# Kernel tuning notes

Measured on AMD Instinct MI355X. Metric: run time of the kernel, lower is better.

Reference implementation:

```python
import jax, jax.numpy as jnp
import numpy as np

# ---- module configuration (from init_kwargs) ----
NX, NV = 2048, 1024
LX = 1.0
VMAX = 6.0
DX = LX / NX
DV = 2.0 * VMAX / NV
XS = jnp.linspace(-LX / 2 + DX / 2, LX / 2 - DX / 2, NX)
VS = jnp.linspace(-VMAX + DV / 2, VMAX - DV / 2, NV)
AE, AI = 1.0, 1836.0
ZE, ZI = -1.0, 1.0
OMEGA_C_TAU = 1.0
NU_EE, NU_II = 1.0, 0.1
DT = 1e-3
T_LBO = 1.0  # LBO temperature, u = 0


def minmod(a, b):
    return jnp.where(a * b > 0, jnp.sign(a) * jnp.minimum(jnp.abs(a), jnp.abs(b)), 0.0)


def _sl(a, lo, hi, axis):
    return jax.lax.slice_in_dim(a, lo, hi, axis=axis)


def slope_limited_flux_divergence(f_pad, F, dx, axis):
    # f_pad has N+4 cells along `axis` (2 ghost cells per side). MUSCL + minmod.
    n = f_pad.shape[axis]
    d = _sl(f_pad, 1, n, axis) - _sl(f_pad, 0, n - 1, axis)          # n-1 diffs
    sigma = minmod(_sl(d, 0, n - 2, axis), _sl(d, 1, n - 1, axis))    # slopes for cells 1..n-2
    fc = _sl(f_pad, 1, n - 1, axis)                                   # cells 1..n-2
    m = n - 2
    fL = _sl(fc, 0, m - 1, axis) + 0.5 * _sl(sigma, 0, m - 1, axis)   # left interface states
    fR = _sl(fc, 1, m, axis) - 0.5 * _sl(sigma, 1, m, axis)           # right interface states
    flux = F(fL, fR)                                                  # N+1 interface fluxes
    k = flux.shape[axis]
    return (_sl(flux, 1, k, axis) - _sl(flux, 0, k - 1, axis)) / dx   # N cells


def pad_x_periodic(f):
    return jnp.concatenate([f[-2:, :], f, f[:2, :]], axis=0)


def pad_v_zero(f):
    z = jnp.zeros((f.shape[0], 2), f.dtype)
    return jnp.concatenate([z, f, z], axis=1)


def poisson_solve(rho_c):
    # dE/dx = rho_c, zero-mean E (periodic-compatible gauge)
    E = jnp.cumsum(rho_c) * DX
    return E - jnp.mean(E)


def species_rhs(f, E, A, Z):
    v = VS[None, :]
    Fx = lambda l, r: jnp.where(v > 0, l * v, r * v)                  # upwind in x
    vdfdx = slope_limited_flux_divergence(pad_x_periodic(f), Fx, DX, axis=0)
    Ec = (OMEGA_C_TAU * Z / A) * E[:, None]
    Fv = lambda l, r: jnp.where(Ec > 0, l * Ec, r * Ec)               # upwind in v
    Edfdv = slope_limited_flux_divergence(pad_v_zero(f), Fv, DV, axis=1)
    return -vdfdx - Edfdv


def vlasov_rhs(fe, fi):
    ne = jnp.sum(fe, axis=1) * DV
    ni = jnp.sum(fi, axis=1) * DV
    E = poisson_solve(ZE * ne + ZI * ni)
    return species_rhs(fe, E, AE, ZE), species_rhs(fi, E, AI, ZI)


def ssprk2(fe, fi, dt):
    re, ri = vlasov_rhs(fe, fi)
    fe1, fi1 = fe + dt * re, fi + dt * ri
    re1, ri1 = vlasov_rhs(fe1, fi1)
    return 0.5 * (fe + fe1 + dt * re1), 0.5 * (fi + fi1 + dt * ri1)


def lbo_diagonals(lam):
    # L f = lam * d/dv( v f + T df/dv ), central differences
    vm = jnp.roll(VS, 1)
    vp = jnp.roll(VS, -1)
    dl = lam * (T_LBO / DV**2 - vm / (2 * DV))
    du = lam * (T_LBO / DV**2 + vp / (2 * DV))
    d = lam * (-2.0 * T_LBO / DV**2) * jnp.ones(NV, XS.dtype)
    return dl.at[0].set(0.0), d, du.at[-1].set(0.0)


def nu_shape():
    midpt = LX / 3
    ef = LX / 6 / 10
    h0 = lambda x: 1 + jnp.exp(x / ef - midpt / ef)
    return 1.0 / (0.5 * (h0(XS) + h0(-XS)))  # [Nx]


def thomas(dl, d, du, b):
    # Thomas algorithm; dl[0]==0 and du[-1]==0 assumed.
    def fwd(carry, inp):
        cp, bp = carry
        dli, di, dui, bi = inp
        m = di - dli * cp
        cpi = dui / m
        bpi = (bi - dli * bp) / m
        return (cpi, bpi), (cpi, bpi)
    z = jnp.zeros((), b.dtype)
    _, (cp, bp) = jax.lax.scan(fwd, (z, z), (dl, d, du, b))
    def bwd(x_next, inp):
        cpi, bpi = inp
        x = bpi - cpi * x_next
        return x, x
    _, x = jax.lax.scan(bwd, z, (cp, bp), reverse=True)
    return x


def implicit_collide(f, lam, dt):
    dl, d, du = lbo_diagonals(lam)
    nu = nu_shape()
    def solve_row(nui, frow):
        return thomas(-dt * nui * dl, 1.0 - dt * nui * d, -dt * nui * du, frow)
    return jax.vmap(solve_row)(nu, f)


def setup_inputs() -> dict:
    key = jax.random.key(0)
    k1, k2 = jax.random.split(key)
    fe = jax.random.uniform(k1, (NX, NV), dtype=jnp.float32)
    fi = jax.random.uniform(k2, (NX, NV), dtype=jnp.float32)
    return {"fe": fe, "fi": fi}


def reference(fe, fi):
    fe1, fi1 = ssprk2(fe, fi, DT)
    fe2 = implicit_collide(fe1, NU_EE, DT)
    fi2 = implicit_collide(fi1, NU_II, DT)
    return jnp.stack([fe2, fi2])  # [2, Nx, Nv]
```

## Files before the change

kernel.cpp:

```cpp
#include <hip/hip_runtime.h>
#include <math.h>

#define NX 2048
#define NV 1024

static constexpr float DXf    = 1.0f / 2048.0f;
static constexpr float DVf    = 12.0f / 1024.0f;
static constexpr float DTf    = 0.001f;
static constexpr float INV_DX = 2048.0f;
static constexpr float INV_DV = 1024.0f / 12.0f;

__device__ __forceinline__ float minmod_f(float a, float b) {
    return __builtin_amdgcn_fmed3f(a, b, 0.0f);
}

__device__ __forceinline__ float frcp(float x) {
    return __builtin_amdgcn_rcpf(x);
}

__device__ __forceinline__ int swz2048(int x) {
    return ((x & 7) << 8) + (x >> 3);
}
__device__ __forceinline__ int swz512(int x) {
    return ((x & 7) << 6) + (x >> 3);
}

__device__ __forceinline__ void rhs4(const float* __restrict__ g, int i, int j0, float Ecs,
                                     float4& f0v, float4& rv) {
    const float* rowc = g + i * NV;
    const float* rm1  = g + (((i - 1) & (NX - 1)) * NV);
    const float* rm2  = g + (((i - 2) & (NX - 1)) * NV);
    const float* rp1  = g + (((i + 1) & (NX - 1)) * NV);
    const float* rp2  = g + (((i + 2) & (NX - 1)) * NV);

    float4 c   = *(const float4*)(rowc + j0);
    float4 xm1 = *(const float4*)(rm1 + j0);
    float4 xm2 = *(const float4*)(rm2 + j0);
    float4 xp1 = *(const float4*)(rp1 + j0);
    float4 xp2 = *(const float4*)(rp2 + j0);
    float4 lm = make_float4(0.f, 0.f, 0.f, 0.f);
    float4 rp = make_float4(0.f, 0.f, 0.f, 0.f);
    if (j0 >= 4)      lm = *(const float4*)(rowc + j0 - 4);
    if (j0 <= NV - 8) rp = *(const float4*)(rowc + j0 + 4);

    float vals[8] = {lm.z, lm.w, c.x, c.y, c.z, c.w, rp.x, rp.y};
    const float* cc   = (const float*)&c;
    const float* am1  = (const float*)&xm1;
    const float* am2  = (const float*)&xm2;
    const float* ap1  = (const float*)&xp1;
    const float* ap2  = (const float*)&xp2;
    float* f0o = (float*)&f0v;
    float* ro  = (float*)&rv;

    #pragma unroll
    for (int k = 0; k < 4; ++k) {
        float f0  = cc[k];
        float fm1 = am1[k], fm2 = am2[k], fp1 = ap1[k], fp2 = ap2[k];

        float vx = (DVf * ((float)(j0 + k) + 0.5f) - 6.0f) * INV_DX;
        float dm1 = fm1 - fm2, d0 = f0 - fm1, dp1 = fp1 - f0, dp2 = fp2 - fp1;
        float sm1 = minmod_f(dm1, d0);
        float s0  = minmod_f(d0, dp1);
        float sp1 = minmod_f(dp1, dp2);
        float selx = (vx > 0.0f) ? (d0 + 0.5f * (s0 - sm1))
                                 : (dp1 - 0.5f * (sp1 - s0));
        float vdfdx = vx * selx;

        float gm2 = vals[k], gm1 = vals[k + 1], gp1 = vals[k + 3], gp2 = vals[k + 4];
        float em1 = gm1 - gm2, e0 = f0 - gm1, ep1 = gp1 - f0, ep2 = gp2 - gp1;
        float tm1 = minmod_f(em1, e0);
        float t0  = minmod_f(e0, ep1);
        float tp1 = minmod_f(ep1, ep2);
        float selv = (Ecs > 0.0f) ? (e0 + 0.5f * (t0 - tm1))
                                  : (ep1 - 0.5f * (tp1 - t0));
        float Edfdv = Ecs * selv;

        f0o[k] = f0;
        ro[k]  = -vdfdx - Edfdv;
    }
}

__global__ __launch_bounds__(256) void moments_kernel(const float* __restrict__ fe,
                                                      const float* __restrict__ fi,
                                                      float* __restrict__ se,
                                                      float* __restrict__ si) {
    const int g = swz512(blockIdx.x);
    const int t = threadIdx.x, lane = t & 63, wv = t >> 6;
    const int row = (g << 2) + wv;
    const float* rpe = fe + (size_t)row * NV;
    const float* rpi = fi + (size_t)row * NV;
    float a = 0.0f, b = 0.0f;
    #pragma unroll
    for (int q = 0; q < 4; ++q) {
        float4 x = *(const float4*)(rpe + 4 * lane + 256 * q);
        float4 y = *(const float4*)(rpi + 4 * lane + 256 * q);
        a += x.x + x.y + x.z + x.w;
        b += y.x + y.y + y.z + y.w;
    }
    #pragma unroll
    for (int off = 32; off > 0; off >>= 1) {
        a += __shfl_down(a, off, 64);
        b += __shfl_down(b, off, 64);
    }
    if (lane == 0) { se[row] = a; si[row] = b; }
}

__global__ __launch_bounds__(256) void escan_kernel(const float* __restrict__ se_,
                                                    const float* __restrict__ si_,
                                                    float* __restrict__ E) {
    const int t = threadIdx.x, lane = t & 63, wv = t >> 6;
    const int k0 = t * 8;
    float4 a0 = *(const float4*)(se_ + k0);
    float4 a1 = *(const float4*)(se_ + k0 + 4);
    float4 b0 = *(const float4*)(si_ + k0);
    float4 b1 = *(const float4*)(si_ + k0 + 4);
    float rho[8];
    rho[0] = DVf * (b0.x - a0.x); rho[1] = DVf * (b0.y - a0.y);
    rho[2] = DVf * (b0.z - a0.z); rho[3] = DVf * (b0.w - a0.w);
    rho[4] = DVf * (b1.x - a1.x); rho[5] = DVf * (b1.y - a1.y);
    rho[6] = DVf * (b1.z - a1.z); rho[7] = DVf * (b1.w - a1.w);
    float s = 0.0f, w = 0.0f;
    #pragma unroll
    for (int r = 0; r < 8; ++r) {
        s += rho[r];
        w += rho[r] * (float)(NX - (k0 + r));
    }
    float sc = s;
    #pragma unroll
    for (int off = 1; off < 64; off <<= 1) {
        float u = __shfl_up(sc, off, 64);
        if (lane >= off) sc += u;
    }
    #pragma unroll
    for (int off = 32; off > 0; off >>= 1) w += __shfl_down(w, off, 64);
    __shared__ float wsum[4], wtot[4];
    if (lane == 63) wsum[wv] = sc;
    if (lane == 0)  wtot[wv] = w;
    __syncthreads();
    float base = 0.0f;
    #pragma unroll
    for (int u = 0; u < 4; ++u) if (u < wv) base += wsum[u];
    float W = wtot[0] + wtot[1] + wtot[2] + wtot[3];
    float run = base + sc - s;
    const float mean = W * (1.0f / (float)NX);
    #pragma unroll
    for (int r = 0; r < 8; ++r) {
        run += rho[r];
        E[k0 + r] = DXf * (run - mean);
    }
}

__global__ __launch_bounds__(256) void stage1_kernel(const float* __restrict__ fe,
                                                     const float* __restrict__ fi,
                                                     const float* __restrict__ E0,
                                                     float* __restrict__ fe1,
                                                     float* __restrict__ fi1,
                                                     float* __restrict__ se1,
                                                     float* __restrict__ si1) {
    const int row = swz2048(blockIdx.x);
    const int sp  = blockIdx.y;
    const float* f = sp ? fi : fe;
    float* f1 = sp ? fi1 : fe1;
    const float zoa = sp ? (1.0f / 1836.0f) : -1.0f;
    const float Ecs = zoa * E0[row] * INV_DV;
    const int t = threadIdx.x, lane = t & 63, wv = t >> 6;
    const int j0 = 4 * t;

    float4 f0v, rv;
    rhs4(f, row, j0, Ecs, f0v, rv);
    float4 o;
    o.x = f0v.x + DTf * rv.x;
    o.y = f0v.y + DTf * rv.y;
    o.z = f0v.z + DTf * rv.z;
    o.w = f0v.w + DTf * rv.w;
    *(float4*)(f1 + (size_t)row * NV + j0) = o;

    float s = o.x + o.y + o.z + o.w;
    #pragma unroll
    for (int off = 32; off > 0; off >>= 1) s += __shfl_down(s, off, 64);
    __shared__ float sred[4];
    if (lane == 0) sred[wv] = s;
    __syncthreads();
    if (t == 0) (sp ? si1 : se1)[row] = sred[0] + sred[1] + sred[2] + sred[3];
}

__global__ __launch_bounds__(256) void stage2_rhs_kernel(const float* __restrict__ fe,
                                                         const float* __restrict__ fi,
                                                         const float* __restrict__ fe1,
                                                         const float* __restrict__ fi1,
                                                         const float* __restrict__ E1,
                                                         float* __restrict__ out) {
    const int row = swz2048(blockIdx.x);
    const int sp  = blockIdx.y;
    const float* h  = sp ? fi : fe;
    const float* f1 = sp ? fi1 : fe1;
    const float zoa = sp ? (1.0f / 1836.0f) : -1.0f;
    const float Ecs = zoa * E1[row] * INV_DV;
    const int t = threadIdx.x;
    const int j0 = 4 * t;
    float* orow = out + ((size_t)sp * NX + row) * NV;

    float4 f0v, rv;
    rhs4(f1, row, j0, Ecs, f0v, rv);
    float4 h4 = *(const float4*)(h + (size_t)row * NV + j0);
    float4 o;
    o.x = 0.5f * h4.x + 0.5f * f0v.x + (0.5f * DTf) * rv.x;
    o.y = 0.5f * h4.y + 0.5f * f0v.y + (0.5f * DTf) * rv.y;
    o.z = 0.5f * h4.z + 0.5f * f0v.z + (0.5f * DTf) * rv.z;
    o.w = 0.5f * h4.w + 0.5f * f0v.w + (0.5f * DTf) * rv.w;
    *(float4*)(orow + j0) = o;
}

__global__ __launch_bounds__(256) void collide_kernel(float* __restrict__ out) {
    const int g  = swz512(blockIdx.x);
    const int sp = blockIdx.y;
    const int t = threadIdx.x, lane = t & 63, wv = t >> 6;
    const int row = (g << 2) + wv;
    const float lam = sp ? 0.1f : 1.0f;
    float* orow = out + ((size_t)sp * NX + row) * NV;

    const float Tdv2   = 1.0f / (DVf * DVf);
    const float inv2dv = 0.5f / DVf;
    const float xi = DXf * ((float)row + 0.5f) - 0.5f;
    const float nu = 1.0f / (1.0f + 0.5f * (expf(60.0f * xi - 20.0f) + expf(-60.0f * xi - 20.0f)));
    const float K = DTf * nu * lam;
    const float b = 1.0f + 2.0f * K * Tdv2;

    const int j0 = 16 * lane;

    float4 q0 = *(const float4*)(orow + j0);
    float4 q1 = *(const float4*)(orow + j0 + 4);
    float4 q2 = *(const float4*)(orow + j0 + 8);
    float4 q3 = *(const float4*)(orow + j0 + 12);
    float d[16] = {q0.x, q0.y, q0.z, q0.w, q1.x, q1.y, q1.z, q1.w,
                   q2.x, q2.y, q2.z, q2.w, q3.x, q3.y, q3.z, q3.w};

    float Dv[16], Av[16], Cv[16];
    #pragma unroll
    for (int r = 0; r < 16; ++r) {
        const int j = j0 + r;
        float a = (j == 0)      ? 0.0f : -K * (Tdv2 - (DVf * ((float)j - 0.5f) - 6.0f) * inv2dv);
        float c = (j == NV - 1) ? 0.0f : -K * (Tdv2 + (DVf * ((float)j + 1.5f) - 6.0f) * inv2dv);
        if (r == 0) {
            float e = frcp(b);
            Dv[0] = e * d[0];
            Av[0] = e * a;
            Cv[0] = e * c;
        } else {
            float e = frcp(b - a * Cv[r - 1]);
            Dv[r] = e * (d[r] - a * Dv[r - 1]);
            Av[r] = -e * a * Av[r - 1];
            Cv[r] = e * c;
        }
    }
    #pragma unroll
    for (int r = 14; r >= 0; --r) {
        Dv[r] = Dv[r] - Cv[r] * Dv[r + 1];
        Av[r] = Av[r] - Cv[r] * Av[r + 1];
        Cv[r] = -Cv[r] * Cv[r + 1];
    }

    float la = Av[0],  ra = Cv[0],  d0 = Dv[0];
    float lb = Av[15], rb = Cv[15], d1 = Dv[15];
    #pragma unroll
    for (int s = 1; s < 64; s <<= 1) {
        float lb_m = __shfl_up(lb, s, 64);
        float rb_m = __shfl_up(rb, s, 64);
        float d1_m = __shfl_up(d1, s, 64);
        if (lane < s) { lb_m = 0.0f; rb_m = 0.0f; d1_m = 0.0f; }
        float la_p = __shfl_down(la, s, 64);
        float ra_p = __shfl_down(ra, s, 64);
        float d0_p = __shfl_down(d0, s, 64);
        if (lane + s > 63) { la_p = 0.0f; ra_p = 0.0f; d0_p = 0.0f; }

        float m00 = 1.0f - la * rb_m;
        float m01 = -ra * la_p;
        float m10 = -lb * rb_m;
        float m11 = 1.0f - rb * la_p;
        float idet = frcp(m00 * m11 - m01 * m10);

        float Lr0 = -la * lb_m, Lr1 = -lb * lb_m;
        float Rr0 = -ra * ra_p, Rr1 = -rb * ra_p;
        float e0 = d0 - la * d1_m - ra * d0_p;
        float e1 = d1 - lb * d1_m - rb * d0_p;

        la = idet * (m11 * Lr0 - m01 * Lr1);
        lb = idet * (m00 * Lr1 - m10 * Lr0);
        ra = idet * (m11 * Rr0 - m01 * Rr1);
        rb = idet * (m00 * Rr1 - m10 * Rr0);
        d0 = idet * (m11 * e0 - m01 * e1);
        d1 = idet * (m00 * e1 - m10 * e0);
    }
    float zl = __shfl_up(d1, 1, 64);
    if (lane == 0) zl = 0.0f;
    float yr = __shfl_down(d0, 1, 64);
    if (lane == 63) yr = 0.0f;

    #pragma unroll
    for (int r = 0; r < 16; ++r) Dv[r] = Dv[r] - Av[r] * zl - Cv[r] * yr;
    #pragma unroll
    for (int q = 0; q < 4; ++q) {
        float4 o;
        o.x = Dv[4 * q + 0];
        o.y = Dv[4 * q + 1];
        o.z = Dv[4 * q + 2];
        o.w = Dv[4 * q + 3];
        *(float4*)(orow + j0 + 4 * q) = o;
    }
}

extern "C" void kernel_launch(void* const* d_in, const int* in_sizes, int n_in,
                              void* d_out, int out_size, void* d_ws, size_t ws_size,
                              hipStream_t stream) {
    const float* fe = (const float*)d_in[0];
    const float* fi = (const float*)d_in[1];
    float* out = (float*)d_out;
    const size_t P = (size_t)NX * NV;

    float* fe1 = (float*)d_ws;
    float* fi1 = fe1 + P;
    float* se  = fi1 + P;
    float* si  = se + NX;
    float* se1 = si + NX;
    float* si1 = se1 + NX;
    float* E0  = si1 + NX;
    float* E1  = E0 + NX;

    dim3 rgrid(2048, 2);
    dim3 qgrid(512, 2);

    moments_kernel<<<512, 256, 0, stream>>>(fe, fi, se, si);
    escan_kernel<<<1, 256, 0, stream>>>(se, si, E0);
    stage1_kernel<<<rgrid, 256, 0, stream>>>(fe, fi, E0, fe1, fi1, se1, si1);
    escan_kernel<<<1, 256, 0, stream>>>(se1, si1, E1);
    stage2_rhs_kernel<<<rgrid, 256, 0, stream>>>(fe, fi, fe1, fi1, E1, out);
    collide_kernel<<<qgrid, 256, 0, stream>>>(out);
}
```

Measured before the change: 105.1 us.

## Fold E-field scan into stage kernels by per-block recomputation of prefix sums

Removes the two single-block escan launches. Each stage block now recomputes its own row's E value from the full 2048-entry moment arrays, using a masked reduction for the prefix and a weighted sum for the mean. This trades two serialized tiny kernels and their launch gaps for redundant reads and reductions of 16 KB in each of 4096 blocks per stage, plus an extra __syncthreads. It also switches expf to __expf in the collision coefficient.

```diff
diff --git a/kernel.cpp b/kernel.cpp
--- a/kernel.cpp
+++ b/kernel.cpp
@@ -25,89 +25,9 @@
     return ((x & 7) << 6) + (x >> 3);
 }
 
-__device__ __forceinline__ void rhs4(const float* __restrict__ g, int i, int j0, float Ecs,
-                                     float4& f0v, float4& rv) {
-    const float* rowc = g + i * NV;
-    const float* rm1  = g + (((i - 1) & (NX - 1)) * NV);
-    const float* rm2  = g + (((i - 2) & (NX - 1)) * NV);
-    const float* rp1  = g + (((i + 1) & (NX - 1)) * NV);
-    const float* rp2  = g + (((i + 2) & (NX - 1)) * NV);
-
-    float4 c   = *(const float4*)(rowc + j0);
-    float4 xm1 = *(const float4*)(rm1 + j0);
-    float4 xm2 = *(const float4*)(rm2 + j0);
-    float4 xp1 = *(const float4*)(rp1 + j0);
-    float4 xp2 = *(const float4*)(rp2 + j0);
-    float4 lm = make_float4(0.f, 0.f, 0.f, 0.f);
-    float4 rp = make_float4(0.f, 0.f, 0.f, 0.f);
-    if (j0 >= 4)      lm = *(const float4*)(rowc + j0 - 4);
-    if (j0 <= NV - 8) rp = *(const float4*)(rowc + j0 + 4);
-
-    float vals[8] = {lm.z, lm.w, c.x, c.y, c.z, c.w, rp.x, rp.y};
-    const float* cc   = (const float*)&c;
-    const float* am1  = (const float*)&xm1;
-    const float* am2  = (const float*)&xm2;
-    const float* ap1  = (const float*)&xp1;
-    const float* ap2  = (const float*)&xp2;
-    float* f0o = (float*)&f0v;
-    float* ro  = (float*)&rv;
-
-    #pragma unroll
-    for (int k = 0; k < 4; ++k) {
-        float f0  = cc[k];
-        float fm1 = am1[k], fm2 = am2[k], fp1 = ap1[k], fp2 = ap2[k];
-
-        float vx = (DVf * ((float)(j0 + k) + 0.5f) - 6.0f) * INV_DX;
-        float dm1 = fm1 - fm2, d0 = f0 - fm1, dp1 = fp1 - f0, dp2 = fp2 - fp1;
-        float sm1 = minmod_f(dm1, d0);
-        float s0  = minmod_f(d0, dp1);
-        float sp1 = minmod_f(dp1, dp2);
-        float selx = (vx > 0.0f) ? (d0 + 0.5f * (s0 - sm1))
-                                 : (dp1 - 0.5f * (sp1 - s0));
-        float vdfdx = vx * selx;
-
-        float gm2 = vals[k], gm1 = vals[k + 1], gp1 = vals[k + 3], gp2 = vals[k + 4];
-        float em1 = gm1 - gm2, e0 = f0 - gm1, ep1 = gp1 - f0, ep2 = gp2 - gp1;
-        float tm1 = minmod_f(em1, e0);
-        float t0  = minmod_f(e0, ep1);
-        float tp1 = minmod_f(ep1, ep2);
-        float selv = (Ecs > 0.0f) ? (e0 + 0.5f * (t0 - tm1))
-                                  : (ep1 - 0.5f * (tp1 - t0));
-        float Edfdv = Ecs * selv;
-
-        f0o[k] = f0;
-        ro[k]  = -vdfdx - Edfdv;
-    }
-}
-
-__global__ __launch_bounds__(256) void moments_kernel(const float* __restrict__ fe,
-                                                      const float* __restrict__ fi,
-                                                      float* __restrict__ se,
-                                                      float* __restrict__ si) {
-    const int g = swz512(blockIdx.x);
-    const int t = threadIdx.x, lane = t & 63, wv = t >> 6;
-    const int row = (g << 2) + wv;
-    const float* rpe = fe + (size_t)row * NV;
-    const float* rpi = fi + (size_t)row * NV;
-    float a = 0.0f, b = 0.0f;
-    #pragma unroll
-    for (int q = 0; q < 4; ++q) {
-        float4 x = *(const float4*)(rpe + 4 * lane + 256 * q);
-        float4 y = *(const float4*)(rpi + 4 * lane + 256 * q);
-        a += x.x + x.y + x.z + x.w;
-        b += y.x + y.y + y.z + y.w;
-    }
-    #pragma unroll
-    for (int off = 32; off > 0; off >>= 1) {
-        a += __shfl_down(a, off, 64);
-        b += __shfl_down(b, off, 64);
-    }
-    if (lane == 0) { se[row] = a; si[row] = b; }
-}
-
-__global__ __launch_bounds__(256) void escan_kernel(const float* __restrict__ se_,
-                                                    const float* __restrict__ si_,
-                                                    float* __restrict__ E) {
+__device__ __forceinline__ float block_E(const float* __restrict__ se_,
+                                         const float* __restrict__ si_,
+                                         int i) {
     const int t = threadIdx.x, lane = t & 63, wv = t >> 6;
     const int k0 = t * 8;
     float4 a0 = *(const float4*)(se_ + k0);
@@ -119,40 +39,110 @@
     rho[2] = DVf * (b0.z - a0.z); rho[3] = DVf * (b0.w - a0.w);
     rho[4] = DVf * (b1.x - a1.x); rho[5] = DVf * (b1.y - a1.y);
     rho[6] = DVf * (b1.z - a1.z); rho[7] = DVf * (b1.w - a1.w);
-    float s = 0.0f, w = 0.0f;
+    float pref = 0.0f, wtot = 0.0f;
     #pragma unroll
     for (int r = 0; r < 8; ++r) {
-        s += rho[r];
-        w += rho[r] * (float)(NX - (k0 + r));
-    }
-    float sc = s;
-    #pragma unroll
-    for (int off = 1; off < 64; off <<= 1) {
-        float u = __shfl_up(sc, off, 64);
-        if (lane >= off) sc += u;
-    }
-    #pragma unroll
-    for (int off = 32; off > 0; off >>= 1) w += __shfl_down(w, off, 64);
-    __shared__ float wsum[4], wtot[4];
-    if (lane == 63) wsum[wv] = sc;
-    if (lane == 0)  wtot[wv] = w;
+        const int k = k0 + r;
+        if (k <= i) pref += rho[r];
+        wtot += rho[r] * (float)(NX - k);
+    }
+    #pragma unroll
+    for (int off = 32; off > 0; off >>= 1) {
+        pref += __shfl_down(pref, off, 64);
+        wtot += __shfl_down(wtot, off, 64);
+    }
+    __shared__ float sp_[4], sw_[4];
+    if (lane == 0) { sp_[wv] = pref; sw_[wv] = wtot; }
     __syncthreads();
-    float base = 0.0f;
-    #pragma unroll
-    for (int u = 0; u < 4; ++u) if (u < wv) base += wsum[u];
-    float W = wtot[0] + wtot[1] + wtot[2] + wtot[3];
-    float run = base + sc - s;
-    const float mean = W * (1.0f / (float)NX);
-    #pragma unroll
-    for (int r = 0; r < 8; ++r) {
-        run += rho[r];
-        E[k0 + r] = DXf * (run - mean);
-    }
+    float P = sp_[0] + sp_[1] + sp_[2] + sp_[3];
+    float W = sw_[0] + sw_[1] + sw_[2] + sw_[3];
+    return DXf * (P - W * (1.0f / (float)NX));
+}
+
+__device__ __forceinline__ void rhs4(const float* __restrict__ g, int i, int j0, float Ecs,
+                                     float4& f0v, float4& rv) {
+    const float* rowc = g + (size_t)i * NV;
+    const float* rm1  = g + (size_t)((i - 1) & (NX - 1)) * NV;
+    const float* rm2  = g + (size_t)((i - 2) & (NX - 1)) * NV;
+    const float* rp1  = g + (size_t)((i + 1) & (NX - 1)) * NV;
+    const float* rp2  = g + (size_t)((i + 2) & (NX - 1)) * NV;
+
+    float4 c   = *(const float4*)(rowc + j0);
+    float4 xm1 = *(const float4*)(rm1 + j0);
+    float4 xm2 = *(const float4*)(rm2 + j0);
+    float4 xp1 = *(const float4*)(rp1 + j0);
+    float4 xp2 = *(const float4*)(rp2 + j0);
+    float4 lm = make_float4(0.f, 0.f, 0.f, 0.f);
+    float4 rp = make_float4(0.f, 0.f, 0.f, 0.f);
+    if (j0 >= 4)      lm = *(const float4*)(rowc + j0 - 4);
+    if (j0 <= NV - 8) rp = *(const float4*)(rowc + j0 + 4);
+
+    float vals[8] = {lm.z, lm.w, c.x, c.y, c.z, c.w, rp.x, rp.y};
+    const float* cc   = (const float*)&c;
+    const float* am1  = (const float*)&xm1;
+    const float* am2  = (const float*)&xm2;
+    const float* ap1  = (const float*)&xp1;
+    const float* ap2  = (const float*)&xp2;
+    float* f0o = (float*)&f0v;
+    float* ro  = (float*)&rv;
+
+    #pragma unroll
+    for (int k = 0; k < 4; ++k) {
+        float f0  = cc[k];
+        float fm1 = am1[k], fm2 = am2[k], fp1 = ap1[k], fp2 = ap2[k];
+
+        float vx = (DVf * ((float)(j0 + k) + 0.5f) - 6.0f) * INV_DX;
+        float dm1 = fm1 - fm2, d0 = f0 - fm1, dp1 = fp1 - f0, dp2 = fp2 - fp1;
+        float sm1 = minmod_f(dm1, d0);
+        float s0  = minmod_f(d0, dp1);
+        float sp1 = minmod_f(dp1, dp2);
+        float selx = (vx > 0.0f) ? (d0 + 0.5f * (s0 - sm1))
+                                 : (dp1 - 0.5f * (sp1 - s0));
+        float vdfdx = vx * selx;
+
+        float gm2 = vals[k], gm1 = vals[k + 1], gp1 = vals[k + 3], gp2 = vals[k + 4];
+        float em1 = gm1 - gm2, e0 = f0 - gm1, ep1 = gp1 - f0, ep2 = gp2 - gp1;
+        float tm1 = minmod_f(em1, e0);
+        float t0  = minmod_f(e0, ep1);
+        float tp1 = minmod_f(ep1, ep2);
+        float selv = (Ecs > 0.0f) ? (e0 + 0.5f * (t0 - tm1))
+                                  : (ep1 - 0.5f * (tp1 - t0));
+        float Edfdv = Ecs * selv;
+
+        f0o[k] = f0;
+        ro[k]  = -vdfdx - Edfdv;
+    }
+}
+
+__global__ __launch_bounds__(256) void moments_kernel(const float* __restrict__ fe,
+                                                      const float* __restrict__ fi,
+                                                      float* __restrict__ se,
+                                                      float* __restrict__ si) {
+    const int g = swz512(blockIdx.x);
+    const int t = threadIdx.x, lane = t & 63, wv = t >> 6;
+    const int row = (g << 2) + wv;
+    const float* rpe = fe + (size_t)row * NV;
+    const float* rpi = fi + (size_t)row * NV;
+    float a = 0.0f, b = 0.0f;
+    #pragma unroll
+    for (int q = 0; q < 4; ++q) {
+        float4 x = *(const float4*)(rpe + 4 * lane + 256 * q);
+        float4 y = *(const float4*)(rpi + 4 * lane + 256 * q);
+        a += x.x + x.y + x.z + x.w;
+        b += y.x + y.y + y.z + y.w;
+    }
+    #pragma unroll
+    for (int off = 32; off > 0; off >>= 1) {
+        a += __shfl_down(a, off, 64);
+        b += __shfl_down(b, off, 64);
+    }
+    if (lane == 0) { se[row] = a; si[row] = b; }
 }
 
 __global__ __launch_bounds__(256) void stage1_kernel(const float* __restrict__ fe,
                                                      const float* __restrict__ fi,
-                                                     const float* __restrict__ E0,
+                                                     const float* __restrict__ se,
+                                                     const float* __restrict__ si,
                                                      float* __restrict__ fe1,
                                                      float* __restrict__ fi1,
                                                      float* __restrict__ se1,
@@ -162,7 +152,7 @@
     const float* f = sp ? fi : fe;
     float* f1 = sp ? fi1 : fe1;
     const float zoa = sp ? (1.0f / 1836.0f) : -1.0f;
-    const float Ecs = zoa * E0[row] * INV_DV;
+    const float Ecs = zoa * block_E(se, si, row) * INV_DV;
     const int t = threadIdx.x, lane = t & 63, wv = t >> 6;
     const int j0 = 4 * t;
 
@@ -188,14 +178,15 @@
                                                          const float* __restrict__ fi,
                                                          const float* __restrict__ fe1,
                                                          const float* __restrict__ fi1,
-                                                         const float* __restrict__ E1,
+                                                         const float* __restrict__ se1,
+                                                         const float* __restrict__ si1,
                                                          float* __restrict__ out) {
     const int row = swz2048(blockIdx.x);
     const int sp  = blockIdx.y;
     const float* h  = sp ? fi : fe;
     const float* f1 = sp ? fi1 : fe1;
     const float zoa = sp ? (1.0f / 1836.0f) : -1.0f;
-    const float Ecs = zoa * E1[row] * INV_DV;
+    const float Ecs = zoa * block_E(se1, si1, row) * INV_DV;
     const int t = threadIdx.x;
     const int j0 = 4 * t;
     float* orow = out + ((size_t)sp * NX + row) * NV;
@@ -222,7 +213,7 @@
     const float Tdv2   = 1.0f / (DVf * DVf);
     const float inv2dv = 0.5f / DVf;
     const float xi = DXf * ((float)row + 0.5f) - 0.5f;
-    const float nu = 1.0f / (1.0f + 0.5f * (expf(60.0f * xi - 20.0f) + expf(-60.0f * xi - 20.0f)));
+    const float nu = 1.0f / (1.0f + 0.5f * (__expf(60.0f * xi - 20.0f) + __expf(-60.0f * xi - 20.0f)));
     const float K = DTf * nu * lam;
     const float b = 1.0f + 2.0f * K * Tdv2;
 
@@ -323,16 +314,12 @@
     float* si  = se + NX;
     float* se1 = si + NX;
     float* si1 = se1 + NX;
-    float* E0  = si1 + NX;
-    float* E1  = E0 + NX;
 
     dim3 rgrid(2048, 2);
     dim3 qgrid(512, 2);
 
     moments_kernel<<<512, 256, 0, stream>>>(fe, fi, se, si);
-    escan_kernel<<<1, 256, 0, stream>>>(se, si, E0);
-    stage1_kernel<<<rgrid, 256, 0, stream>>>(fe, fi, E0, fe1, fi1, se1, si1);
-    escan_kernel<<<1, 256, 0, stream>>>(se1, si1, E1);
-    stage2_rhs_kernel<<<rgrid, 256, 0, stream>>>(fe, fi, fe1, fi1, E1, out);
+    stage1_kernel<<<rgrid, 256, 0, stream>>>(fe, fi, se, si, fe1, fi1, se1, si1);
+    stage2_rhs_kernel<<<rgrid, 256, 0, stream>>>(fe, fi, fe1, fi1, se1, si1, out);
     collide_kernel<<<qgrid, 256, 0, stream>>>(out);
 }
```

Measured after the change: 104.7 us. No clear change (-0.3%).
